# Kernel tuning notes

Hardware: AMD Instinct MI355X
Metric: run time of the kernel (lower is better)

The kernel has to match this reference:

```python
import jax, jax.numpy as jnp
import numpy as np

EPS = 1e-5
KS = 3  # deformable kernel size
K2 = KS * KS


def conv2d(x, w, stride=1, padding=1):
    return jax.lax.conv_general_dilated(
        x, w, window_strides=(stride, stride),
        padding=[(padding, padding), (padding, padding)],
        dimension_numbers=("NCHW", "OIHW", "NCHW"))


def batchnorm(x, gamma, beta):
    # training-mode BN: batch statistics over (N, H, W)
    mean = jnp.mean(x, axis=(0, 2, 3), keepdims=True)
    var = jnp.var(x, axis=(0, 2, 3), keepdims=True)
    xhat = (x - mean) * jax.lax.rsqrt(var + EPS)
    return xhat * gamma[None, :, None, None] + beta[None, :, None, None]


def deform_conv(x, offsets, w, pad=1):
    # x: (B,C,H,W); offsets: (B,2*K2,H,W) -> first K2 channels = row (y)
    # offsets, next K2 = col (x) offsets; w: (O,C,KS,KS)
    B, C, H, W = x.shape
    xp = jnp.pad(x, ((0, 0), (0, 0), (pad, pad), (pad, pad)))
    Hp, Wp = H + 2 * pad, W + 2 * pad
    # base grid (center of each output pixel in padded coords)
    p0_y = jnp.arange(H, dtype=x.dtype) + pad            # (H,)
    p0_x = jnp.arange(W, dtype=x.dtype) + pad            # (W,)
    # kernel tap offsets in [-1, 0, 1]^2, row-major
    pn = jnp.stack(jnp.meshgrid(jnp.arange(KS) - pad, jnp.arange(KS) - pad,
                                indexing="ij"), axis=-1).reshape(K2, 2).astype(x.dtype)
    off = offsets.reshape(B, 2, K2, H, W)
    off_y = jnp.transpose(off[:, 0], (0, 2, 3, 1))       # (B,H,W,K2)
    off_x = jnp.transpose(off[:, 1], (0, 2, 3, 1))
    py = p0_y[None, :, None, None] + pn[:, 0][None, None, None, :] + off_y
    px = p0_x[None, None, :, None] + pn[:, 1][None, None, None, :] + off_x
    py = jnp.clip(py, 0.0, Hp - 1.0)
    px = jnp.clip(px, 0.0, Wp - 1.0)
    y0 = jnp.floor(py).astype(jnp.int32)
    x0 = jnp.floor(px).astype(jnp.int32)
    y1 = jnp.minimum(y0 + 1, Hp - 1)
    x1 = jnp.minimum(x0 + 1, Wp - 1)
    wy = (py - y0.astype(x.dtype))[:, None]              # (B,1,H,W,K2)
    wx = (px - x0.astype(x.dtype))[:, None]

    def gather(xb, yi, xi):                              # xb (C,Hp,Wp)
        return xb[:, yi, xi]                             # (C,H,W,K2)
    g = jax.vmap(gather)
    v00 = g(xp, y0, x0)
    v01 = g(xp, y0, x1)
    v10 = g(xp, y1, x0)
    v11 = g(xp, y1, x1)
    sampled = (v00 * (1 - wy) * (1 - wx) + v01 * (1 - wy) * wx +
               v10 * wy * (1 - wx) + v11 * wy * wx)      # (B,C,H,W,K2)
    return jnp.einsum("bchwk,ock->bohw", sampled, w.reshape(w.shape[0], C, K2))


def setup_inputs() -> dict:
    key = jax.random.key(0)
    ks = jax.random.split(key, 16)
    B, Cin, P, H, W = 64, 64, 64, 64, 64
    s = lambda k, shp, fan: jax.random.normal(k, shp, jnp.float32) * (fan ** -0.5)
    return {
        "x": jax.random.normal(ks[0], (B, Cin, H, W), jnp.float32),
        "conv1_w": s(ks[1], (P, Cin, 3, 3), Cin * 9),
        "bn1_g": jnp.ones((P,), jnp.float32), "bn1_b": jnp.zeros((P,), jnp.float32),
        "conv2_w": s(ks[2], (16, P, 1, 1), P),
        "bn2_g": jnp.ones((16,), jnp.float32), "bn2_b": jnp.zeros((16,), jnp.float32),
        "off_w": s(ks[3], (18, 16, 3, 3), 16 * 9) * 0.1,
        "off_b": jnp.zeros((18,), jnp.float32),
        "conv3_w": s(ks[4], (16, 16, 3, 3), 16 * 9),
        "bn3_g": jnp.ones((16,), jnp.float32), "bn3_b": jnp.zeros((16,), jnp.float32),
        "conv4_w": s(ks[5], (P, 16, 3, 3), 16 * 9),
        "bn4_g": jnp.ones((P,), jnp.float32), "bn4_b": jnp.zeros((P,), jnp.float32),
    }


def reference(x, conv1_w, bn1_g, bn1_b, conv2_w, bn2_g, bn2_b, off_w, off_b,
              conv3_w, bn3_g, bn3_b, conv4_w, bn4_g, bn4_b):
    out = jax.nn.relu(batchnorm(conv2d(x, conv1_w, 1, 1), bn1_g, bn1_b))
    out = jax.nn.relu(batchnorm(conv2d(out, conv2_w, 1, 0), bn2_g, bn2_b))
    offsets = conv2d(out, off_w, 1, 1) + off_b[None, :, None, None]
    out = jax.nn.relu(batchnorm(deform_conv(out, offsets, conv3_w), bn3_g, bn3_b))
    out = batchnorm(conv2d(out, conv4_w, 1, 1), bn4_g, bn4_b)
    out = out + x  # identity shortcut (stride=1, in_planes==planes)
    return jax.nn.relu(out)
```

## Files before the change

kernel.cpp:

```cpp
#include <hip/hip_runtime.h>

#define BN_N 262144.0f

typedef unsigned short u16;
typedef __attribute__((ext_vector_type(8))) short short8;
typedef __attribute__((ext_vector_type(4))) float floatx4;

#define RP1 4224
#define IS1 278784
#define RP2 1584
#define IS2 104544
#define H2P_TOTAL 6690816

static __device__ __forceinline__ u16 f2bf(float f) {
  union { float f; unsigned u; } v; v.f = f;
  unsigned u = v.u;
  return (u16)((u + 0x7FFFu + ((u >> 16) & 1u)) >> 16);
}
static __device__ __forceinline__ float bf2f(u16 h) {
  union { unsigned u; float f; } v; v.u = ((unsigned)h) << 16;
  return v.f;
}
static __device__ __forceinline__ void cp16(const u16* g, u16* l) {
  __builtin_amdgcn_global_load_lds((const __attribute__((address_space(1))) unsigned int*)g,
                                   (__attribute__((address_space(3))) unsigned int*)l, 16, 0, 0);
}

__global__ __launch_bounds__(256) void prep_w_k(const float* __restrict__ w1,
                                                u16* __restrict__ Bsw) {
  int d = blockIdx.x * 256 + threadIdx.x;
  int kin = d & 7, n = (d >> 3) & 63, kgrp = (d >> 9) & 3, kc = d >> 11;
  int k = kc * 32 + kgrp * 8 + kin;
  int tap = k >> 6, c = k & 63;
  Bsw[d] = f2bf(w1[n * 576 + c * 9 + tap]);
}

__global__ __launch_bounds__(256) void prep_w4_k(const float* __restrict__ w4,
                                                 u16* __restrict__ Bsw4) {
  int d = blockIdx.x * 256 + threadIdx.x;
  if (d >= 10240) return;
  int kin = d & 7, n = (d >> 3) & 63, lk = (d >> 9) & 3, kk = d >> 11;
  int tap = kk * 2 + (lk >> 1);
  int c = ((lk & 1) << 3) + kin;
  float v = (tap < 9) ? w4[n * 144 + c * 9 + tap] : 0.f;
  Bsw4[d] = f2bf(v);
}

__global__ __launch_bounds__(256) void prep_w3_k(const float* __restrict__ w3,
                                                 u16* __restrict__ Bsw3) {
  int d = blockIdx.x * 256 + threadIdx.x;
  if (d >= 2560) return;
  int kin = d & 7, n = (d >> 3) & 15, lk = (d >> 7) & 3, kk = d >> 9;
  int k = kk * 32 + lk * 8 + kin;
  int tap = k >> 4, c = k & 15;
  float v = (tap < 9) ? w3[n * 144 + c * 9 + tap] : 0.f;
  Bsw3[d] = f2bf(v);
}

__global__ __launch_bounds__(256) void prep_wo_k(const float* __restrict__ ow,
                                                 u16* __restrict__ BswO) {
  int d = blockIdx.x * 256 + threadIdx.x;
  if (d >= 5120) return;
  int kin = d & 7, n = (d >> 3) & 31, lk = (d >> 8) & 3, kk = d >> 10;
  int tap = kk * 2 + (lk >> 1);
  int c = ((lk & 1) << 3) + kin;
  float v = (tap < 9 && n < 18) ? ow[n * 144 + c * 9 + tap] : 0.f;
  BswO[d] = f2bf(v);
}

__global__ __launch_bounds__(256) void prep_x_k(const float* __restrict__ x,
                                                u16* __restrict__ xp) {
  int yp = blockIdx.x;
  int b = blockIdx.y;
  int tid = threadIdx.x;
  u16* rowbase = xp + (size_t)(b * 66 + yp) * RP1;
  if (yp == 0 || yp == 65) {
    for (int i = tid; i < RP1 / 4; i += 256)
      ((ushort4*)rowbase)[i] = make_ushort4(0, 0, 0, 0);
    return;
  }
  int y = yp - 1;
  __shared__ __align__(16) u16 s[64][72];
  for (int i = tid; i < 4096; i += 256) {
    int c = i >> 6, xx = i & 63;
    s[xx][c] = f2bf(x[((b * 64 + c) << 12) + (y << 6) + xx]);
  }
  if (tid < 128) {
    int c = tid & 63;
    int pxp = (tid >> 6) ? 65 : 0;
    rowbase[pxp * 64 + c] = 0;
  }
  __syncthreads();
  for (int j = tid; j < 512; j += 256) {
    int xx = j >> 3, chunk = j & 7;
    int pxp = xx + 1;
    int ph = chunk ^ (pxp & 7);
    *(short8*)(rowbase + pxp * 64 + ph * 8) = *(const short8*)(&s[xx][chunk * 8]);
  }
}

__global__ __launch_bounds__(256, 1) void conv1_mfma(const u16* __restrict__ xp,
                                                     const u16* __restrict__ Bsw,
                                                     u16* __restrict__ h1,
                                                     float* __restrict__ sum1, float* __restrict__ sq1) {
  __shared__ __align__(16) u16 ring[43520];
  __shared__ __align__(16) u16 lB[36864];
  __shared__ float LSQ[512];
  const int tid = threadIdx.x;
  const int w = tid >> 6, l = tid & 63;
  const int lm = l & 15, lk = l >> 4;
  const int b = blockIdx.x >> 2;
  const int quarter = blockIdx.x & 3;
  const int c0 = quarter * 8;
  const u16* xb = xp + (size_t)b * 66 * RP1;

  for (int i = w; i < 72; i += 4) cp16(Bsw + i * 512 + l * 8, lB + i * 512);
#pragma unroll
  for (int c = 0; c < 3; ++c) {
    const u16* src = xb + (size_t)(2 * (c0 + c)) * RP1;
    u16* dst = ring + ((c0 + c) % 5) * 8704;
    for (int s = w; s < 17; s += 4) cp16(src + s * 512 + l * 8, dst + s * 512);
  }
  asm volatile("s_waitcnt vmcnt(0)" ::: "memory");
  __builtin_amdgcn_s_barrier();
  __builtin_amdgcn_sched_barrier(0);

  float ssum[4] = {0.f, 0.f, 0.f, 0.f}, sqsm[4] = {0.f, 0.f, 0.f, 0.f};

#pragma unroll 1
  for (int j = 0; j < 4; ++j) {
    const int y0 = quarter * 16 + j * 4;
    if (j < 3) {
#pragma unroll
      for (int c = 0; c < 2; ++c) {
        const int ch = c0 + 2 * j + 3 + c;
        const u16* src = xb + (size_t)(2 * ch) * RP1;
        u16* dst = ring + (ch % 5) * 8704;
        for (int s = w; s < 17; s += 4) cp16(src + s * 512 + l * 8, dst + s * 512);
      }
      __builtin_amdgcn_sched_barrier(0);
    }

    floatx4 acc[4][4];
#pragma unroll
    for (int mt = 0; mt < 4; ++mt)
#pragma unroll
      for (int nb = 0; nb < 4; ++nb)
        acc[mt][nb] = (floatx4){0.f, 0.f, 0.f, 0.f};

#pragma unroll
    for (int kk = 0; kk < 18; ++kk) {
      const int tap = kk >> 1;
      const int dy = (tap < 3) ? 0 : ((tap < 6) ? 1 : 2);
      const int dx = tap - dy * 3;
      const int chunk16 = ((kk & 1) << 2) + lk;
      const int pr = y0 + w + dy;
      const u16* abase = ring + ((pr >> 1) % 5) * 8704 + (pr & 1) * 4224;
      short8 aF[4], bF[4];
      const u16* bp = lB + (((kk * 4 + lk) * 64) + lm) * 8;
      bF[0] = *(const short8*)(bp);
      bF[1] = *(const short8*)(bp + 128);
      bF[2] = *(const short8*)(bp + 256);
      bF[3] = *(const short8*)(bp + 384);
#pragma unroll
      for (int mt = 0; mt < 4; ++mt) {
        int pxp = mt * 16 + lm + dx;
        int ph = chunk16 ^ (pxp & 7);
        aF[mt] = *(const short8*)(abase + pxp * 64 + ph * 8);
      }
#pragma unroll
      for (int mt = 0; mt < 4; ++mt)
#pragma unroll
        for (int nb = 0; nb < 4; ++nb)
          acc[mt][nb] = __builtin_amdgcn_mfma_f32_16x16x32_bf16(aF[mt], bF[nb], acc[mt][nb], 0, 0, 0);
    }

    const int y = y0 + w;
#pragma unroll
    for (int mt = 0; mt < 4; ++mt)
#pragma unroll
      for (int nb = 0; nb < 4; ++nb) {
        u16* dst = h1 + ((size_t)(b * 64 + nb * 16 + lm) << 12) + (y << 6) + mt * 16 + (lk << 2);
        floatx4 v = acc[mt][nb];
        *(ushort4*)dst = make_ushort4(f2bf(v.x), f2bf(v.y), f2bf(v.z), f2bf(v.w));
      }

#pragma unroll
    for (int nb = 0; nb < 4; ++nb)
#pragma unroll
      for (int mt = 0; mt < 4; ++mt) {
        floatx4 a = acc[mt][nb];
        ssum[nb] += a.x + a.y + a.z + a.w;
        sqsm[nb] += a.x * a.x + a.y * a.y + a.z * a.z + a.w * a.w;
      }

    if (j < 3) {
      asm volatile("s_waitcnt vmcnt(16)" ::: "memory");
      __builtin_amdgcn_s_barrier();
      __builtin_amdgcn_sched_barrier(0);
    }
  }

  float* LS = LSQ;
  float* LQ = LSQ + 256;
#pragma unroll
  for (int nb = 0; nb < 4; ++nb) {
    ssum[nb] += __shfl_xor(ssum[nb], 16, 64);  ssum[nb] += __shfl_xor(ssum[nb], 32, 64);
    sqsm[nb] += __shfl_xor(sqsm[nb], 16, 64);  sqsm[nb] += __shfl_xor(sqsm[nb], 32, 64);
  }
  if (lk == 0) {
#pragma unroll
    for (int nb = 0; nb < 4; ++nb) { LS[w * 64 + nb * 16 + lm] = ssum[nb]; LQ[w * 64 + nb * 16 + lm] = sqsm[nb]; }
  }
  __syncthreads();
  if (tid < 64) atomicAdd(&sum1[tid], LS[tid] + LS[64 + tid] + LS[128 + tid] + LS[192 + tid]);
  else if (tid < 128) { int o = tid - 64; atomicAdd(&sq1[o], LQ[o] + LQ[64 + o] + LQ[128 + o] + LQ[192 + o]); }
}

__global__ __launch_bounds__(256) void conv2_k(const u16* __restrict__ h1,
                                               const float* __restrict__ w2,
                                               const float* __restrict__ sum1, const float* __restrict__ sq1,
                                               const float* __restrict__ g1, const float* __restrict__ b1,
                                               float* __restrict__ out,
                                               float* __restrict__ sum2, float* __restrict__ sq2) {
  __shared__ float s_wt[64 * 16];
  __shared__ float s_scale[64], s_shift[64];
  __shared__ float ls[4][16], lsq[4][16];
  int tid = threadIdx.x;
  for (int i = tid; i < 1024; i += 256) {
    int o = i >> 6, c = i & 63;
    s_wt[c * 16 + o] = w2[i];
  }
  if (tid < 64) {
    float m = sum1[tid] / BN_N;
    float var = sq1[tid] / BN_N - m * m;
    float sc = g1[tid] * rsqrtf(var + 1e-5f);
    s_scale[tid] = sc;
    s_shift[tid] = b1[tid] - m * sc;
  }
  __syncthreads();
  int p = blockIdx.x * 256 + tid;
  int b = p >> 12, r = p & 4095;
  const u16* src = h1 + ((size_t)b << 18) + r;
  float acc[16];
#pragma unroll
  for (int o = 0; o < 16; ++o) acc[o] = 0.f;
  for (int c = 0; c < 64; ++c) {
    float v = bf2f(src[c << 12]);
    v = fmaxf(v * s_scale[c] + s_shift[c], 0.f);
    const float* wp = &s_wt[c * 16];
    float4 w0 = *(const float4*)wp;
    float4 w1 = *(const float4*)(wp + 4);
    float4 w2v = *(const float4*)(wp + 8);
    float4 w3v = *(const float4*)(wp + 12);
    acc[0] += w0.x * v;  acc[1] += w0.y * v;  acc[2] += w0.z * v;  acc[3] += w0.w * v;
    acc[4] += w1.x * v;  acc[5] += w1.y * v;  acc[6] += w1.z * v;  acc[7] += w1.w * v;
    acc[8] += w2v.x * v; acc[9] += w2v.y * v; acc[10] += w2v.z * v; acc[11] += w2v.w * v;
    acc[12] += w3v.x * v; acc[13] += w3v.y * v; acc[14] += w3v.z * v; acc[15] += w3v.w * v;
  }
  float* dst = out + (size_t)p * 16;
#pragma unroll
  for (int c4 = 0; c4 < 4; ++c4)
    *(float4*)(dst + c4 * 4) = make_float4(acc[c4*4], acc[c4*4+1], acc[c4*4+2], acc[c4*4+3]);
  int lane = tid & 63, wv = tid >> 6;
#pragma unroll
  for (int o = 0; o < 16; ++o) {
    float s = acc[o], s2 = acc[o] * acc[o];
#pragma unroll
    for (int off = 32; off > 0; off >>= 1) {
      s += __shfl_down(s, off, 64);
      s2 += __shfl_down(s2, off, 64);
    }
    if (lane == 0) { ls[wv][o] = s; lsq[wv][o] = s2; }
  }
  __syncthreads();
  if (tid < 16) atomicAdd(&sum2[tid], ls[0][tid] + ls[1][tid] + ls[2][tid] + ls[3][tid]);
  else if (tid < 32) {
    int o = tid - 16;
    atomicAdd(&sq2[o], lsq[0][o] + lsq[1][o] + lsq[2][o] + lsq[3][o]);
  }
}

__global__ __launch_bounds__(256) void bnrelu2_k(const float* __restrict__ ws2,
                                                 const float* __restrict__ sum2, const float* __restrict__ sq2,
                                                 const float* __restrict__ g2, const float* __restrict__ b2,
                                                 u16* __restrict__ h2p) {
  __shared__ float s_scale[16], s_shift[16];
  int tid = threadIdx.x;
  if (tid < 16) {
    float m = sum2[tid] / BN_N;
    float var = sq2[tid] / BN_N - m * m;
    float sc = g2[tid] * rsqrtf(var + 1e-5f);
    s_scale[tid] = sc;
    s_shift[tid] = b2[tid] - m * sc;
  }
  __syncthreads();
  int p = blockIdx.x * 256 + tid;
  int b = p >> 12, r = p & 4095;
  int y = r >> 6, xx = r & 63;
  const float* src = ws2 + (size_t)p * 16;
  u16* dst = h2p + (size_t)(b * 66 + y + 1) * RP2 + (xx + 1) * 24;
#pragma unroll
  for (int c4 = 0; c4 < 4; ++c4) {
    float4 v = *(const float4*)(src + c4 * 4);
    u16 o0 = f2bf(fmaxf(v.x * s_scale[c4*4]   + s_shift[c4*4],   0.f));
    u16 o1 = f2bf(fmaxf(v.y * s_scale[c4*4+1] + s_shift[c4*4+1], 0.f));
    u16 o2 = f2bf(fmaxf(v.z * s_scale[c4*4+2] + s_shift[c4*4+2], 0.f));
    u16 o3 = f2bf(fmaxf(v.w * s_scale[c4*4+3] + s_shift[c4*4+3], 0.f));
    *(ushort4*)(dst + c4 * 4) = make_ushort4(o0, o1, o2, o3);
  }
}

__global__ __launch_bounds__(256) void offconv_mfma(const u16* __restrict__ h2p,
                                                    const u16* __restrict__ BswO,
                                                    const float* __restrict__ ob,
                                                    float* __restrict__ offs) {
  __shared__ __align__(16) u16 lA[9728];
  __shared__ __align__(16) u16 lB[5120];
  const int tid = threadIdx.x;
  const int w = tid >> 6, l = tid & 63;
  const int lm = l & 15, lk = l >> 4;
  const int b = blockIdx.x >> 4;
  const int y0 = (blockIdx.x & 15) << 2;
  const int y = y0 + w;
  const u16* src = h2p + ((size_t)b * 66 + y0) * RP2;
  for (int seg = w; seg < 19; seg += 4) cp16(src + seg * 512 + l * 8, lA + seg * 512);
  for (int seg = w; seg < 10; seg += 4) cp16(BswO + seg * 512 + l * 8, lB + seg * 512);
  __syncthreads();

  floatx4 acc[4][2];
#pragma unroll
  for (int mt = 0; mt < 4; ++mt)
#pragma unroll
    for (int nb = 0; nb < 2; ++nb)
      acc[mt][nb] = (floatx4){0.f, 0.f, 0.f, 0.f};

#pragma unroll
  for (int kk = 0; kk < 5; ++kk) {
    int tap = kk * 2 + (lk >> 1);
    if (tap > 8) tap = 8;
    const int dy = tap / 3, dx = tap - dy * 3;
    const int c0 = (lk & 1) << 3;
    const int rowoff = (w + dy) * RP2;
    short8 aF[4], bF[2];
#pragma unroll
    for (int mt = 0; mt < 4; ++mt)
      aF[mt] = *(const short8*)(lA + rowoff + (mt * 16 + lm + dx) * 24 + c0);
    const u16* bp = lB + (((kk * 4 + lk) * 32) + lm) * 8;
    bF[0] = *(const short8*)(bp);
    bF[1] = *(const short8*)(bp + 128);
#pragma unroll
    for (int mt = 0; mt < 4; ++mt)
#pragma unroll
      for (int nb = 0; nb < 2; ++nb)
        acc[mt][nb] = __builtin_amdgcn_mfma_f32_16x16x32_bf16(aF[mt], bF[nb], acc[mt][nb], 0, 0, 0);
  }

#pragma unroll
  for (int mt = 0; mt < 4; ++mt)
#pragma unroll
    for (int nb = 0; nb < 2; ++nb) {
      int oc = nb * 16 + lm;
      if (oc < 18) {
        float bias = ob[oc];
        floatx4 v = acc[mt][nb];
        v.x += bias; v.y += bias; v.z += bias; v.w += bias;
        float* dst = offs + (size_t)b * 73728 + (oc << 12) + (y << 6) + mt * 16 + (lk << 2);
        *(floatx4*)dst = v;
      }
    }
}

__global__ __launch_bounds__(256) void deform_mfma(const u16* __restrict__ h2p,
                                                   const float* __restrict__ offs,
                                                   const u16* __restrict__ Bsw3,
                                                   float* __restrict__ out,
                                                   float* __restrict__ sum3, float* __restrict__ sq3) {
  const int tid = threadIdx.x;
  const int w = tid >> 6, l = tid & 63;
  const int lm = l & 15, lk = l >> 4;
  const int pbase = blockIdx.x * 256 + w * 64;
  const int b = pbase >> 12;
  const u16* img = h2p + (size_t)b * IS2;
  const float* offp = offs + (size_t)b * 73728;

  short8 bf[5];
#pragma unroll
  for (int kk = 0; kk < 5; ++kk)
    bf[kk] = *(const short8*)(Bsw3 + (((kk * 4 + lk) * 16) + lm) * 8);

  floatx4 acc[4];
#pragma unroll
  for (int mt = 0; mt < 4; ++mt) acc[mt] = (floatx4){0.f, 0.f, 0.f, 0.f};

#pragma unroll
  for (int mt = 0; mt < 4; ++mt) {
    const int p = pbase + mt * 16 + lm;
    const int r = p & 4095;
    const int y = r >> 6, x = r & 63;
#pragma unroll
    for (int kk = 0; kk < 5; ++kk) {
      const int k0 = kk * 32 + lk * 8;
      int tap = k0 >> 4;
      const int c0 = k0 & 15;
      if (tap > 8) tap = 8;
      const int dy = tap / 3, dx = tap - dy * 3;
      float offy = offp[(tap << 12) + r];
      float offx = offp[((tap + 9) << 12) + r];
      float py = (float)(y + dy) + offy;
      float px = (float)(x + dx) + offx;
      py = fminf(fmaxf(py, 0.f), 65.f);
      px = fminf(fmaxf(px, 0.f), 65.f);
      float y0f = floorf(py), x0f = floorf(px);
      int y0 = (int)y0f, x0 = (int)x0f;
      int y1 = min(y0 + 1, 65), x1 = min(x0 + 1, 65);
      float wy = py - y0f, wx = px - x0f;
      float w00 = (1.f - wy) * (1.f - wx), w01 = (1.f - wy) * wx;
      float w10 = wy * (1.f - wx),         w11 = wy * wx;
      short8 v00 = *(const short8*)(img + (y0 * 66 + x0) * 24 + c0);
      short8 v01 = *(const short8*)(img + (y0 * 66 + x1) * 24 + c0);
      short8 v10 = *(const short8*)(img + (y1 * 66 + x0) * 24 + c0);
      short8 v11 = *(const short8*)(img + (y1 * 66 + x1) * 24 + c0);
      short8 a;
#pragma unroll
      for (int j = 0; j < 8; ++j) {
        float s = bf2f((u16)v00[j]) * w00 + bf2f((u16)v01[j]) * w01
                + bf2f((u16)v10[j]) * w10 + bf2f((u16)v11[j]) * w11;
        a[j] = (short)f2bf(s);
      }
      acc[mt] = __builtin_amdgcn_mfma_f32_16x16x32_bf16(a, bf[kk], acc[mt], 0, 0, 0);
    }
  }

  float s = 0.f, s2 = 0.f;
#pragma unroll
  for (int mt = 0; mt < 4; ++mt) {
    floatx4 a = acc[mt];
    s += a.x + a.y + a.z + a.w;
    s2 += a.x * a.x + a.y * a.y + a.z * a.z + a.w * a.w;
#pragma unroll
    for (int reg = 0; reg < 4; ++reg) {
      int pp = pbase + mt * 16 + lk * 4 + reg;
      out[(size_t)pp * 16 + lm] = acc[mt][reg];
    }
  }
  __shared__ float ls[4][16], lsq[4][16];
  s += __shfl_xor(s, 16, 64);  s += __shfl_xor(s, 32, 64);
  s2 += __shfl_xor(s2, 16, 64); s2 += __shfl_xor(s2, 32, 64);
  if (lk == 0) { ls[w][lm] = s; lsq[w][lm] = s2; }
  __syncthreads();
  if (tid < 16) atomicAdd(&sum3[tid], ls[0][tid] + ls[1][tid] + ls[2][tid] + ls[3][tid]);
  else if (tid < 32) {
    int o = tid - 16;
    atomicAdd(&sq3[o], lsq[0][o] + lsq[1][o] + lsq[2][o] + lsq[3][o]);
  }
}

__global__ __launch_bounds__(256) void bnrelu3_k(const float* __restrict__ wsd,
                                                 const float* __restrict__ sum3, const float* __restrict__ sq3,
                                                 const float* __restrict__ g3, const float* __restrict__ b3,
                                                 u16* __restrict__ h3p) {
  __shared__ float s_scale[16], s_shift[16];
  int tid = threadIdx.x;
  if (tid < 16) {
    float m = sum3[tid] / BN_N;
    float var = sq3[tid] / BN_N - m * m;
    float sc = g3[tid] * rsqrtf(var + 1e-5f);
    s_scale[tid] = sc;
    s_shift[tid] = b3[tid] - m * sc;
  }
  __syncthreads();
  int p = blockIdx.x * 256 + tid;
  int b = p >> 12, r = p & 4095;
  int y = r >> 6, xx = r & 63;
  const float* src = wsd + (size_t)p * 16;
  u16* dst = h3p + (size_t)(b * 66 + y + 1) * RP2 + (xx + 1) * 24;
#pragma unroll
  for (int c4 = 0; c4 < 4; ++c4) {
    float4 v = *(const float4*)(src + c4 * 4);
    u16 o0 = f2bf(fmaxf(v.x * s_scale[c4*4]   + s_shift[c4*4],   0.f));
    u16 o1 = f2bf(fmaxf(v.y * s_scale[c4*4+1] + s_shift[c4*4+1], 0.f));
    u16 o2 = f2bf(fmaxf(v.z * s_scale[c4*4+2] + s_shift[c4*4+2], 0.f));
    u16 o3 = f2bf(fmaxf(v.w * s_scale[c4*4+3] + s_shift[c4*4+3], 0.f));
    *(ushort4*)(dst + c4 * 4) = make_ushort4(o0, o1, o2, o3);
  }
}

__global__ __launch_bounds__(256) void conv4_mfma(const u16* __restrict__ h3p,
                                                  const u16* __restrict__ Bsw4,
                                                  u16* __restrict__ h4,
                                                  float* __restrict__ sum4, float* __restrict__ sq4) {
  __shared__ __align__(16) u16 lA[9728];
  __shared__ __align__(16) u16 lB[10240];
  const int tid = threadIdx.x;
  const int w = tid >> 6, l = tid & 63;
  const int lm = l & 15, lk = l >> 4;
  const int b = blockIdx.x >> 4;
  const int y0 = (blockIdx.x & 15) << 2;
  const int y = y0 + w;
  const u16* src = h3p + ((size_t)b * 66 + y0) * RP2;
  for (int seg = w; seg < 19; seg += 4) cp16(src + seg * 512 + l * 8, lA + seg * 512);
  for (int seg = w; seg < 20; seg += 4) cp16(Bsw4 + seg * 512 + l * 8, lB + seg * 512);
  __syncthreads();

  floatx4 acc[4][4];
#pragma unroll
  for (int mt = 0; mt < 4; ++mt)
#pragma unroll
    for (int nb = 0; nb < 4; ++nb)
      acc[mt][nb] = (floatx4){0.f, 0.f, 0.f, 0.f};

#pragma unroll
  for (int kk = 0; kk < 5; ++kk) {
    int tap = kk * 2 + (lk >> 1);
    if (tap > 8) tap = 8;
    const int dy = tap / 3, dx = tap - dy * 3;
    const int c0 = (lk & 1) << 3;
    const int rowoff = (w + dy) * RP2;
    short8 aF[4], bF[4];
#pragma unroll
    for (int mt = 0; mt < 4; ++mt)
      aF[mt] = *(const short8*)(lA + rowoff + (mt * 16 + lm + dx) * 24 + c0);
    const u16* bp = lB + (((kk * 4 + lk) * 64) + lm) * 8;
    bF[0] = *(const short8*)(bp);
    bF[1] = *(const short8*)(bp + 128);
    bF[2] = *(const short8*)(bp + 256);
    bF[3] = *(const short8*)(bp + 384);
#pragma unroll
    for (int mt = 0; mt < 4; ++mt)
#pragma unroll
      for (int nb = 0; nb < 4; ++nb)
        acc[mt][nb] = __builtin_amdgcn_mfma_f32_16x16x32_bf16(aF[mt], bF[nb], acc[mt][nb], 0, 0, 0);
  }

#pragma unroll
  for (int mt = 0; mt < 4; ++mt)
#pragma unroll
    for (int nb = 0; nb < 4; ++nb) {
      u16* dst = h4 + ((size_t)(b * 64 + nb * 16 + lm) << 12) + (y << 6) + mt * 16 + (lk << 2);
      floatx4 v = acc[mt][nb];
      *(ushort4*)dst = make_ushort4(f2bf(v.x), f2bf(v.y), f2bf(v.z), f2bf(v.w));
    }

  __syncthreads();
  float* LS = (float*)lA;
  float* LQ = LS + 256;
  float s[4], s2[4];
#pragma unroll
  for (int nb = 0; nb < 4; ++nb) {
    s[nb] = 0.f; s2[nb] = 0.f;
#pragma unroll
    for (int mt = 0; mt < 4; ++mt) {
      floatx4 a = acc[mt][nb];
      s[nb] += a.x + a.y + a.z + a.w;
      s2[nb] += a.x * a.x + a.y * a.y + a.z * a.z + a.w * a.w;
    }
    s[nb] += __shfl_xor(s[nb], 16, 64);  s[nb] += __shfl_xor(s[nb], 32, 64);
    s2[nb] += __shfl_xor(s2[nb], 16, 64); s2[nb] += __shfl_xor(s2[nb], 32, 64);
  }
  if (lk == 0) {
#pragma unroll
    for (int nb = 0; nb < 4; ++nb) { LS[w * 64 + nb * 16 + lm] = s[nb]; LQ[w * 64 + nb * 16 + lm] = s2[nb]; }
  }
  __syncthreads();
  if (tid < 64) atomicAdd(&sum4[tid], LS[tid] + LS[64 + tid] + LS[128 + tid] + LS[192 + tid]);
  else if (tid < 128) { int o = tid - 64; atomicAdd(&sq4[o], LQ[o] + LQ[64 + o] + LQ[128 + o] + LQ[192 + o]); }
}

__global__ __launch_bounds__(256) void final_k(const u16* __restrict__ h4,
                                               float* __restrict__ out,
                                               const float* __restrict__ x,
                                               const float* __restrict__ sum4, const float* __restrict__ sq4,
                                               const float* __restrict__ g4, const float* __restrict__ b4) {
  __shared__ float s_scale[64], s_shift[64];
  int tid = threadIdx.x;
  if (tid < 64) {
    float m = sum4[tid] / BN_N;
    float var = sq4[tid] / BN_N - m * m;
    float sc = g4[tid] * rsqrtf(var + 1e-5f);
    s_scale[tid] = sc;
    s_shift[tid] = b4[tid] - m * sc;
  }
  __syncthreads();
  int i = (blockIdx.x * 256 + tid) * 4;
  int c = (i >> 12) & 63;
  ushort4 q = *(const ushort4*)(h4 + i);
  float4 xv = *(const float4*)(x + i);
  float sc = s_scale[c], sh = s_shift[c];
  float4 v;
  v.x = fmaxf(bf2f(q.x) * sc + sh + xv.x, 0.f);
  v.y = fmaxf(bf2f(q.y) * sc + sh + xv.y, 0.f);
  v.z = fmaxf(bf2f(q.z) * sc + sh + xv.z, 0.f);
  v.w = fmaxf(bf2f(q.w) * sc + sh + xv.w, 0.f);
  *(float4*)(out + i) = v;
}

extern "C" void kernel_launch(void* const* d_in, const int* in_sizes, int n_in,
                              void* d_out, int out_size, void* d_ws, size_t ws_size,
                              hipStream_t stream) {
  const float* x  = (const float*)d_in[0];
  const float* w1 = (const float*)d_in[1];
  const float* g1 = (const float*)d_in[2];
  const float* b1 = (const float*)d_in[3];
  const float* w2 = (const float*)d_in[4];
  const float* g2 = (const float*)d_in[5];
  const float* b2 = (const float*)d_in[6];
  const float* ow = (const float*)d_in[7];
  const float* ob = (const float*)d_in[8];
  const float* w3 = (const float*)d_in[9];
  const float* g3 = (const float*)d_in[10];
  const float* b3 = (const float*)d_in[11];
  const float* w4 = (const float*)d_in[12];
  const float* g4 = (const float*)d_in[13];
  const float* b4 = (const float*)d_in[14];
  float* out = (float*)d_out;
  float* ws = (float*)d_ws;

  float* offs = ws;
  float* wsd  = offs + 4718592;
  float* ws2  = wsd + 4194304;
  float* h2pf = ws2 + 4194304;
  float* stats = h2pf + 4460544;
  float* sum1 = stats, *sq1 = stats + 64;
  float* sum2 = stats + 128, *sq2 = stats + 144;
  float* sum3 = stats + 160, *sq3 = stats + 176;
  float* sum4 = stats + 192, *sq4 = stats + 256;
  u16* xp   = (u16*)ws;
  u16* Bsw  = (u16*)(stats + 320);
  u16* Bsw4 = Bsw + 36864;
  u16* Bsw3 = Bsw4 + 10240;
  u16* BswO = Bsw3 + 2560;
  u16* h2p  = (u16*)h2pf;
  u16* h4   = (u16*)offs;
  u16* h1   = (u16*)out;

  hipMemsetAsync(stats, 0, 320 * sizeof(float), stream);
  hipMemsetAsync(h2p, 0, (size_t)H2P_TOTAL * sizeof(u16), stream);

  prep_w_k<<<144, 256, 0, stream>>>(w1, Bsw);
  prep_w4_k<<<40, 256, 0, stream>>>(w4, Bsw4);
  prep_w3_k<<<10, 256, 0, stream>>>(w3, Bsw3);
  prep_wo_k<<<20, 256, 0, stream>>>(ow, BswO);
  prep_x_k<<<dim3(66, 64), 256, 0, stream>>>(x, xp);
  conv1_mfma<<<256, 256, 0, stream>>>(xp, Bsw, h1, sum1, sq1);
  conv2_k<<<1024, 256, 0, stream>>>(h1, w2, sum1, sq1, g1, b1, ws2, sum2, sq2);
  bnrelu2_k<<<1024, 256, 0, stream>>>(ws2, sum2, sq2, g2, b2, h2p);
  offconv_mfma<<<1024, 256, 0, stream>>>(h2p, BswO, ob, offs);
  deform_mfma<<<1024, 256, 0, stream>>>(h2p, offs, Bsw3, wsd, sum3, sq3);
  bnrelu3_k<<<1024, 256, 0, stream>>>(wsd, sum3, sq3, g3, b3, h2p );
  conv4_mfma<<<1024, 256, 0, stream>>>(h2p, Bsw4, h4, sum4, sq4);
  final_k<<<16384, 256, 0, stream>>>(h4, out, x, sum4, sq4, g4, b4);
}
```

Measured before the change: 323.8 us.

## Merge weight-prep kernels and split conv1 output channels across 8 waves

```diff
diff --git a/kernel.cpp b/kernel.cpp
--- a/kernel.cpp
+++ b/kernel.cpp
@@ -26,46 +26,41 @@
                                    (__attribute__((address_space(3))) unsigned int*)l, 16, 0, 0);
 }
 
-__global__ __launch_bounds__(256) void prep_w_k(const float* __restrict__ w1,
-                                                u16* __restrict__ Bsw) {
-  int d = blockIdx.x * 256 + threadIdx.x;
-  int kin = d & 7, n = (d >> 3) & 63, kgrp = (d >> 9) & 3, kc = d >> 11;
-  int k = kc * 32 + kgrp * 8 + kin;
-  int tap = k >> 6, c = k & 63;
-  Bsw[d] = f2bf(w1[n * 576 + c * 9 + tap]);
-}
-
-__global__ __launch_bounds__(256) void prep_w4_k(const float* __restrict__ w4,
-                                                 u16* __restrict__ Bsw4) {
-  int d = blockIdx.x * 256 + threadIdx.x;
-  if (d >= 10240) return;
-  int kin = d & 7, n = (d >> 3) & 63, lk = (d >> 9) & 3, kk = d >> 11;
-  int tap = kk * 2 + (lk >> 1);
-  int c = ((lk & 1) << 3) + kin;
-  float v = (tap < 9) ? w4[n * 144 + c * 9 + tap] : 0.f;
-  Bsw4[d] = f2bf(v);
-}
-
-__global__ __launch_bounds__(256) void prep_w3_k(const float* __restrict__ w3,
-                                                 u16* __restrict__ Bsw3) {
-  int d = blockIdx.x * 256 + threadIdx.x;
-  if (d >= 2560) return;
-  int kin = d & 7, n = (d >> 3) & 15, lk = (d >> 7) & 3, kk = d >> 9;
-  int k = kk * 32 + lk * 8 + kin;
-  int tap = k >> 4, c = k & 15;
-  float v = (tap < 9) ? w3[n * 144 + c * 9 + tap] : 0.f;
-  Bsw3[d] = f2bf(v);
-}
-
-__global__ __launch_bounds__(256) void prep_wo_k(const float* __restrict__ ow,
-                                                 u16* __restrict__ BswO) {
-  int d = blockIdx.x * 256 + threadIdx.x;
-  if (d >= 5120) return;
-  int kin = d & 7, n = (d >> 3) & 31, lk = (d >> 8) & 3, kk = d >> 10;
-  int tap = kk * 2 + (lk >> 1);
-  int c = ((lk & 1) << 3) + kin;
-  float v = (tap < 9 && n < 18) ? ow[n * 144 + c * 9 + tap] : 0.f;
-  BswO[d] = f2bf(v);
+__global__ __launch_bounds__(256) void prep_weights_k(const float* __restrict__ w1,
+                                                      const float* __restrict__ w4,
+                                                      const float* __restrict__ w3,
+                                                      const float* __restrict__ ow,
+                                                      u16* __restrict__ Bsw, u16* __restrict__ Bsw4,
+                                                      u16* __restrict__ Bsw3, u16* __restrict__ BswO) {
+  int blk = blockIdx.x, tid = threadIdx.x;
+  if (blk < 144) {
+    int d = blk * 256 + tid;
+    int kin = d & 7, n = (d >> 3) & 63, kgrp = (d >> 9) & 3, kc = d >> 11;
+    int k = kc * 32 + kgrp * 8 + kin;
+    int tap = k >> 6, c = k & 63;
+    Bsw[d] = f2bf(w1[n * 576 + c * 9 + tap]);
+  } else if (blk < 184) {
+    int d = (blk - 144) * 256 + tid;
+    int kin = d & 7, n = (d >> 3) & 63, lkk = (d >> 9) & 3, kk = d >> 11;
+    int tap = kk * 2 + (lkk >> 1);
+    int c = ((lkk & 1) << 3) + kin;
+    float v = (tap < 9) ? w4[n * 144 + c * 9 + tap] : 0.f;
+    Bsw4[d] = f2bf(v);
+  } else if (blk < 194) {
+    int d = (blk - 184) * 256 + tid;
+    int kin = d & 7, n = (d >> 3) & 15, lkk = (d >> 7) & 3, kk = d >> 9;
+    int k = kk * 32 + lkk * 8 + kin;
+    int tap = k >> 4, c = k & 15;
+    float v = (tap < 9) ? w3[n * 144 + c * 9 + tap] : 0.f;
+    Bsw3[d] = f2bf(v);
+  } else {
+    int d = (blk - 194) * 256 + tid;
+    int kin = d & 7, n = (d >> 3) & 31, lkk = (d >> 8) & 3, kk = d >> 10;
+    int tap = kk * 2 + (lkk >> 1);
+    int c = ((lkk & 1) << 3) + kin;
+    float v = (tap < 9 && n < 18) ? ow[n * 144 + c * 9 + tap] : 0.f;
+    BswO[d] = f2bf(v);
+  }
 }
 
 __global__ __launch_bounds__(256) void prep_x_k(const float* __restrict__ x,
@@ -99,33 +94,39 @@
   }
 }
 
-__global__ __launch_bounds__(256, 1) void conv1_mfma(const u16* __restrict__ xp,
+__global__ __launch_bounds__(512, 2) void conv1_mfma(const u16* __restrict__ xp,
                                                      const u16* __restrict__ Bsw,
                                                      u16* __restrict__ h1,
                                                      float* __restrict__ sum1, float* __restrict__ sq1) {
   __shared__ __align__(16) u16 ring[43520];
-  __shared__ __align__(16) u16 lB[36864];
-  __shared__ float LSQ[512];
+  __shared__ float LS[256], LQ[256];
   const int tid = threadIdx.x;
-  const int w = tid >> 6, l = tid & 63;
+  const int w8 = tid >> 6, l = tid & 63;
+  const int r = w8 & 3, g = w8 >> 2;
   const int lm = l & 15, lk = l >> 4;
   const int b = blockIdx.x >> 2;
   const int quarter = blockIdx.x & 3;
   const int c0 = quarter * 8;
   const u16* xb = xp + (size_t)b * 66 * RP1;
 
-  for (int i = w; i < 72; i += 4) cp16(Bsw + i * 512 + l * 8, lB + i * 512);
+  short8 bReg[18][2];
+#pragma unroll
+  for (int kk = 0; kk < 18; ++kk)
+#pragma unroll
+    for (int j = 0; j < 2; ++j)
+      bReg[kk][j] = *(const short8*)(Bsw + (((kk * 4 + lk) * 64) + (g * 2 + j) * 16 + lm) * 8);
+
 #pragma unroll
   for (int c = 0; c < 3; ++c) {
     const u16* src = xb + (size_t)(2 * (c0 + c)) * RP1;
     u16* dst = ring + ((c0 + c) % 5) * 8704;
-    for (int s = w; s < 17; s += 4) cp16(src + s * 512 + l * 8, dst + s * 512);
+    for (int s = w8; s < 17; s += 8) cp16(src + s * 512 + l * 8, dst + s * 512);
   }
   asm volatile("s_waitcnt vmcnt(0)" ::: "memory");
   __builtin_amdgcn_s_barrier();
   __builtin_amdgcn_sched_barrier(0);
 
-  float ssum[4] = {0.f, 0.f, 0.f, 0.f}, sqsm[4] = {0.f, 0.f, 0.f, 0.f};
+  float ssum[2] = {0.f, 0.f}, sqsm[2] = {0.f, 0.f};
 
 #pragma unroll 1
   for (int j = 0; j < 4; ++j) {
@@ -136,16 +137,16 @@
         const int ch = c0 + 2 * j + 3 + c;
         const u16* src = xb + (size_t)(2 * ch) * RP1;
         u16* dst = ring + (ch % 5) * 8704;
-        for (int s = w; s < 17; s += 4) cp16(src + s * 512 + l * 8, dst + s * 512);
+        for (int s = w8; s < 17; s += 8) cp16(src + s * 512 + l * 8, dst + s * 512);
       }
       __builtin_amdgcn_sched_barrier(0);
     }
 
-    floatx4 acc[4][4];
+    floatx4 acc[4][2];
 #pragma unroll
     for (int mt = 0; mt < 4; ++mt)
 #pragma unroll
-      for (int nb = 0; nb < 4; ++nb)
+      for (int nb = 0; nb < 2; ++nb)
         acc[mt][nb] = (floatx4){0.f, 0.f, 0.f, 0.f};
 
 #pragma unroll
@@ -154,14 +155,9 @@
       const int dy = (tap < 3) ? 0 : ((tap < 6) ? 1 : 2);
       const int dx = tap - dy * 3;
       const int chunk16 = ((kk & 1) << 2) + lk;
-      const int pr = y0 + w + dy;
+      const int pr = y0 + r + dy;
       const u16* abase = ring + ((pr >> 1) % 5) * 8704 + (pr & 1) * 4224;
-      short8 aF[4], bF[4];
-      const u16* bp = lB + (((kk * 4 + lk) * 64) + lm) * 8;
-      bF[0] = *(const short8*)(bp);
-      bF[1] = *(const short8*)(bp + 128);
-      bF[2] = *(const short8*)(bp + 256);
-      bF[3] = *(const short8*)(bp + 384);
+      short8 aF[4];
 #pragma unroll
       for (int mt = 0; mt < 4; ++mt) {
         int pxp = mt * 16 + lm + dx;
@@ -171,22 +167,23 @@
 #pragma unroll
       for (int mt = 0; mt < 4; ++mt)
 #pragma unroll
-        for (int nb = 0; nb < 4; ++nb)
-          acc[mt][nb] = __builtin_amdgcn_mfma_f32_16x16x32_bf16(aF[mt], bF[nb], acc[mt][nb], 0, 0, 0);
-    }
-
-    const int y = y0 + w;
+        for (int nb = 0; nb < 2; ++nb)
+          acc[mt][nb] = __builtin_amdgcn_mfma_f32_16x16x32_bf16(aF[mt], bReg[kk][nb], acc[mt][nb], 0, 0, 0);
+    }
+
+    const int y = y0 + r;
 #pragma unroll
     for (int mt = 0; mt < 4; ++mt)
 #pragma unroll
-      for (int nb = 0; nb < 4; ++nb) {
-        u16* dst = h1 + ((size_t)(b * 64 + nb * 16 + lm) << 12) + (y << 6) + mt * 16 + (lk << 2);
+      for (int nb = 0; nb < 2; ++nb) {
+        const int oc = g * 32 + nb * 16 + lm;
+        u16* dst = h1 + ((size_t)(b * 64 + oc) << 12) + (y << 6) + mt * 16 + (lk << 2);
         floatx4 v = acc[mt][nb];
         *(ushort4*)dst = make_ushort4(f2bf(v.x), f2bf(v.y), f2bf(v.z), f2bf(v.w));
       }
 
 #pragma unroll
-    for (int nb = 0; nb < 4; ++nb)
+    for (int nb = 0; nb < 2; ++nb)
 #pragma unroll
       for (int mt = 0; mt < 4; ++mt) {
         floatx4 a = acc[mt][nb];
@@ -195,22 +192,23 @@
       }
 
     if (j < 3) {
-      asm volatile("s_waitcnt vmcnt(16)" ::: "memory");
+      asm volatile("s_waitcnt vmcnt(8)" ::: "memory");
       __builtin_amdgcn_s_barrier();
       __builtin_amdgcn_sched_barrier(0);
     }
   }
 
-  float* LS = LSQ;
-  float* LQ = LSQ + 256;
-#pragma unroll
-  for (int nb = 0; nb < 4; ++nb) {
+#pragma unroll
+  for (int nb = 0; nb < 2; ++nb) {
     ssum[nb] += __shfl_xor(ssum[nb], 16, 64);  ssum[nb] += __shfl_xor(ssum[nb], 32, 64);
     sqsm[nb] += __shfl_xor(sqsm[nb], 16, 64);  sqsm[nb] += __shfl_xor(sqsm[nb], 32, 64);
   }
   if (lk == 0) {
 #pragma unroll
-    for (int nb = 0; nb < 4; ++nb) { LS[w * 64 + nb * 16 + lm] = ssum[nb]; LQ[w * 64 + nb * 16 + lm] = sqsm[nb]; }
+    for (int nb = 0; nb < 2; ++nb) {
+      const int oc = g * 32 + nb * 16 + lm;
+      LS[r * 64 + oc] = ssum[nb];  LQ[r * 64 + oc] = sqsm[nb];
+    }
   }
   __syncthreads();
   if (tid < 64) atomicAdd(&sum1[tid], LS[tid] + LS[64 + tid] + LS[128 + tid] + LS[192 + tid]);
@@ -637,12 +635,9 @@
   hipMemsetAsync(stats, 0, 320 * sizeof(float), stream);
   hipMemsetAsync(h2p, 0, (size_t)H2P_TOTAL * sizeof(u16), stream);
 
-  prep_w_k<<<144, 256, 0, stream>>>(w1, Bsw);
-  prep_w4_k<<<40, 256, 0, stream>>>(w4, Bsw4);
-  prep_w3_k<<<10, 256, 0, stream>>>(w3, Bsw3);
-  prep_wo_k<<<20, 256, 0, stream>>>(ow, BswO);
+  prep_weights_k<<<214, 256, 0, stream>>>(w1, w4, w3, ow, Bsw, Bsw4, Bsw3, BswO);
   prep_x_k<<<dim3(66, 64), 256, 0, stream>>>(x, xp);
-  conv1_mfma<<<256, 256, 0, stream>>>(xp, Bsw, h1, sum1, sq1);
+  conv1_mfma<<<256, 512, 0, stream>>>(xp, Bsw, h1, sum1, sq1);
   conv2_k<<<1024, 256, 0, stream>>>(h1, w2, sum1, sq1, g1, b1, ws2, sum2, sq2);
   bnrelu2_k<<<1024, 256, 0, stream>>>(ws2, sum2, sq2, g2, b2, h2p);
   offconv_mfma<<<1024, 256, 0, stream>>>(h2p, BswO, ob, offs);
```

Measured after the change: 317.1 us. -2.1%, faster.
